# Kernel tuning notes

Measured on AMD Instinct MI355X. Metric: run time of the kernel, lower is better.

The kernel has to match this reference:

```python
import jax, jax.numpy as jnp
import numpy as np
from jax import lax

DX, DY, T, B, NMC, HID = 128, 64, 50, 128, 100, 64
PROC_SD, EMIT_SD, LOC_R = 0.05, 0.1, 5.0


def gaspari_cohn(radius, d):
    # static construction (numpy), matches construct_Gaspari_Cohn
    def G(z):
        if 0 <= z < 1:
            return 1.0 - 5.0/3*z**2 + 5.0/8*z**3 + 0.5*z**4 - 0.25*z**5
        elif 1 <= z < 2:
            return 4.0 - 5.0*z + 5.0/3*z**2 + 5.0/8*z**3 - 0.5*z**4 + 1.0/12*z**5 - 2.0/(3.0*z)
        return 0.0
    t = np.zeros((d, d), dtype=np.float32)
    for i in range(d):
        for j in range(d):
            dist = min(abs(i - j), d - abs(i - j))
            t[i, j] = G(dist / radius)
    return jnp.asarray(t)


def setup_inputs():
    key = jax.random.key(0)
    ks = jax.random.split(key, 16)
    rn = lambda k, s, sc=0.05: (jax.random.normal(k, s) * sc).astype(jnp.float32)
    return {
        'observations': jax.random.normal(ks[0], (B, T, DY), jnp.float32),
        'W1': rn(ks[1], (128, DX)), 'b1': jnp.zeros((128,), jnp.float32),
        'W2': rn(ks[2], (64, 128)), 'b2': jnp.zeros((64,), jnp.float32),
        'W3': rn(ks[3], (32, 64)), 'b3': jnp.zeros((32,), jnp.float32),
        'W4': rn(ks[4], (DX, 32)), 'b4': jnp.zeros((DX,), jnp.float32),
        'Wih': rn(ks[5], (4 * HID, DY)), 'Whh': rn(ks[6], (4 * HID, HID)), 'bih': jnp.zeros((4 * HID,), jnp.float32),
        'Wm': rn(ks[7], (DX, HID)), 'bm': jnp.zeros((DX,), jnp.float32),
        'Wv': rn(ks[8], (DX, HID)), 'bv': jnp.zeros((DX,), jnp.float32),
        'eps0': jax.random.normal(ks[9], (NMC, B, DX), jnp.float32),
        'eps_seq': jax.random.normal(ks[10], (T, NMC, B, DX), jnp.float32),
        'noise_y': jax.random.normal(ks[11], (T, B, DY), jnp.float32),
    }


def _forward(observations, W1, b1, W2, b2, W3, b3, W4, b4,
             Wih, Whh, bih, Wm, bm, Wv, bv, eps0, eps_seq, noise_y):
    dt = observations.dtype
    taper = gaspari_cohn(LOC_R, DX).astype(dt)        # [dx, dx]
    Hm = jnp.eye(DX, dtype=dt)[:DY]                    # [dy, dx] emission matrix
    R = (EMIT_SD ** 2) * jnp.eye(DY, dtype=dt)         # observation noise cov

    def mlp(x):  # Four_Layer_NN, relu, no residual
        h = jax.nn.relu(x @ W1.T + b1)
        h = jax.nn.relu(h @ W2.T + b2)
        h = jax.nn.relu(h @ W3.T + b3)
        return h @ W4.T + b4

    # ---- LSTM recognition net -> q(x0) (diagonal MVN) ----
    def lstm_step(carry, x_t):
        h, c = carry
        g = x_t @ Wih.T + h @ Whh.T + bih
        i, f, gg, o = jnp.split(g, 4, axis=-1)
        c = jax.nn.sigmoid(f) * c + jax.nn.sigmoid(i) * jnp.tanh(gg)
        h = jax.nn.sigmoid(o) * jnp.tanh(c)
        return (h, c), None
    h0 = jnp.zeros((B, HID), dt)
    (h_last, _), _ = lax.scan(lstm_step, (h0, h0), jnp.moveaxis(observations, 1, 0))
    q_mean = h_last @ Wm.T + bm                          # [B, dx]
    q_var = jax.nn.softplus(h_last @ Wv.T + bv) + 1e-4   # [B, dx]

    # KL[ q(x0) || N(0, I) ], diagonal covariance
    kl = 0.5 * jnp.sum(q_var + q_mean ** 2 - 1.0 - jnp.log(q_var), axis=-1).mean()

    # rsample ensemble x0: [NMC, B, dx]
    x0 = q_mean[None] + jnp.sqrt(q_var)[None] * eps0

    log2pi = jnp.log(2 * jnp.asarray(np.pi, dt))

    def enkf_step(x_prev, inp):
        y_t, eps_t, ny_t = inp                            # [B,dy], [NMC,B,dx], [B,dy]
        # NN prediction + process noise
        x_t = mlp(x_prev) + eps_t * PROC_SD               # [NMC, B, dx]
        X = jnp.moveaxis(x_t, 0, 1)                       # [B, NMC, dx]
        Xm = X.mean(axis=1, keepdims=True)                # [B, 1, dx]
        Xc = X - Xm
        # localized ensemble covariance (var_inflation = 0)
        P = taper * (jnp.einsum('bnd,bne->bde', Xc, Xc) / (NMC - 1))  # [B, dx, dx]
        # perturbed observations (chol(R) diagonal)
        y_pert = y_t + ny_t * EMIT_SD                     # [B, dy]
        HX = jnp.einsum('bnd,od->bno', X, Hm)             # [B, NMC, dy]
        HP = jnp.einsum('od,bde->boe', Hm, P)             # [B, dy, dx]
        S = jnp.einsum('boe,pe->bop', HP, Hm) + R         # [B, dy, dy]
        L = jnp.linalg.cholesky(S)
        K = jax.scipy.linalg.cho_solve((L, True), HP)     # [B, dy, dx] = S^-1 HP
        X_post = X + jnp.einsum('bno,boe->bne', y_pert[:, None, :] - HX, K)
        HXm = jnp.einsum('bkd,od->bko', Xm, Hm)           # [B, 1, dy]
        Xm_post = Xm + jnp.einsum('bko,boe->bke', y_t[:, None, :] - HXm, K)
        # EnKF marginal log-likelihood N(y | H Xm, S)
        r = y_t - HXm[:, 0, :]
        z = jax.scipy.linalg.solve_triangular(L, r[..., None], lower=True)[..., 0]
        ll = (-0.5 * jnp.sum(z ** 2, -1)
              - jnp.sum(jnp.log(jnp.diagonal(L, axis1=-2, axis2=-1)), -1)
              - 0.5 * DY * log2pi)
        return jnp.moveaxis(X_post, 0, 1), (ll.mean(), Xm_post[:, 0, :])

    xs = (jnp.moveaxis(observations, 1, 0), eps_seq, noise_y)
    _, (lls, means) = lax.scan(enkf_step, x0, xs)
    elbo = -kl + jnp.sum(lls)
    return elbo, means  # means: [T, B, dx] posterior ensemble means


def reference(observations, W1, b1, W2, b2, W3, b3, W4, b4,
              Wih, Whh, bih, Wm, bm, Wv, bv, eps0, eps_seq, noise_y):
    return _forward(observations, W1, b1, W2, b2, W3, b3, W4, b4,
                    Wih, Whh, bih, Wm, bm, Wv, bv, eps0, eps_seq, noise_y)
```

## Files before the change

### kernel.cpp

```cpp
#include <hip/hip_runtime.h>

#define TC   50
#define BC   128
#define DXC  128
#define DYC  64
#define NMCC 100
#define XBS  136
#define A1S  136
#define A2S  72
#define A3S  40
#define IVS  72
#define KTS  72
#define HPS  20
#define LBS  12
#define ZSS  67
#define W2S  136
#define W3S  72

typedef float f32x4 __attribute__((ext_vector_type(4)));
typedef short s16x8 __attribute__((ext_vector_type(8)));

__device__ __forceinline__ unsigned short f2bf(float x){
  unsigned int u = __float_as_uint(x);
  u += 0x7fffu + ((u >> 16) & 1u);
  return (unsigned short)(u >> 16);
}

__device__ __forceinline__ unsigned int pk2bf(float lo, float hi){
  unsigned int r;
  asm volatile("v_cvt_pk_bf16_f32 %0, %1, %2" : "=v"(r) : "v"(lo), "v"(hi));
  return r;
}

__device__ __forceinline__ f32x4 mfma16(s16x8 a, s16x8 b, f32x4 c){
  return __builtin_amdgcn_mfma_f32_16x16x32_bf16(a, b, c, 0, 0, 0);
}

__device__ __forceinline__ s16x8 packA8(const float* p){
  f32x4 a = *(const f32x4*)p;
  f32x4 c = *(const f32x4*)(p + 4);
  s16x8 r;
  r[0]=(short)f2bf(a[0]); r[1]=(short)f2bf(a[1]);
  r[2]=(short)f2bf(a[2]); r[3]=(short)f2bf(a[3]);
  r[4]=(short)f2bf(c[0]); r[5]=(short)f2bf(c[1]);
  r[6]=(short)f2bf(c[2]); r[7]=(short)f2bf(c[3]);
  return r;
}

__device__ __forceinline__ float gc_taper(int row, int col){
  int dd = row - col; if (dd < 0) dd = -dd;
  if (128 - dd < dd) dd = 128 - dd;
  double z = (double)dd / 5.0;
  double g = 0.0;
  if (z < 1.0){
    g = 1.0 - (5.0/3.0)*z*z + (5.0/8.0)*z*z*z + 0.5*z*z*z*z - 0.25*z*z*z*z*z;
  } else if (z < 2.0){
    g = 4.0 - 5.0*z + (5.0/3.0)*z*z + (5.0/8.0)*z*z*z - 0.5*z*z*z*z
        + (1.0/12.0)*z*z*z*z*z - 2.0/(3.0*z);
  }
  return (float)(g / 99.0);
}

__global__ __launch_bounds__(256) void gin_kernel(const float* __restrict__ obs,
                          const float* __restrict__ Wih, const float* __restrict__ bih,
                          float* __restrict__ gin){
  __shared__ float xrow[64];
  int blk = blockIdx.x;
  int t = blk / BC, b = blk % BC;
  int tid = threadIdx.x;
  if (tid < 64) xrow[tid] = obs[(b*TC + t)*DYC + tid];
  __syncthreads();
  float s = bih[tid];
  #pragma unroll
  for (int k = 0; k < 64; k += 4){
    f32x4 wv = *(const f32x4*)&Wih[tid*64 + k];
    s += wv[0]*xrow[k] + wv[1]*xrow[k+1] + wv[2]*xrow[k+2] + wv[3]*xrow[k+3];
  }
  gin[blk*256 + tid] = s;
}

__global__ __launch_bounds__(256,1) void lstm_kernel(const float* __restrict__ gin,
     const float* __restrict__ Whh,
     const float* __restrict__ Wm, const float* __restrict__ bm,
     const float* __restrict__ Wv, const float* __restrict__ bv,
     float* __restrict__ qmean, float* __restrict__ qstd, float* __restrict__ klp){
  __shared__ float h[64], cc[64], graw[256], red[128];
  int b = blockIdx.x, tid = threadIdx.x;
  float w[64];
  #pragma unroll
  for (int k = 0; k < 64; k += 4){
    f32x4 v = *(const f32x4*)&Whh[tid*64 + k];
    w[k]=v[0]; w[k+1]=v[1]; w[k+2]=v[2]; w[k+3]=v[3];
  }
  if (tid < 64){ h[tid] = 0.f; cc[tid] = 0.f; }
  __syncthreads();
  for (int t = 0; t < TC; ++t){
    float g = gin[(t*BC + b)*256 + tid];
    #pragma unroll
    for (int k = 0; k < 64; k += 4){
      f32x4 hv = *(const f32x4*)&h[k];
      g += hv[0]*w[k] + hv[1]*w[k+1] + hv[2]*w[k+2] + hv[3]*w[k+3];
    }
    graw[tid] = g;
    __syncthreads();
    if (tid < 64){
      float ig = 1.f/(1.f + expf(-graw[tid]));
      float fg = 1.f/(1.f + expf(-graw[64 + tid]));
      float gg = tanhf(graw[128 + tid]);
      float og = 1.f/(1.f + expf(-graw[192 + tid]));
      float cn = fg*cc[tid] + ig*gg;
      cc[tid] = cn;
      h[tid] = og*tanhf(cn);
    }
    __syncthreads();
  }
  if (tid < 128){
    float sm_ = bm[tid], sv_ = bv[tid];
    #pragma unroll
    for (int k = 0; k < 64; k += 4){
      f32x4 wmv = *(const f32x4*)&Wm[tid*64 + k];
      f32x4 wvv = *(const f32x4*)&Wv[tid*64 + k];
      f32x4 hv  = *(const f32x4*)&h[k];
      sm_ += wmv[0]*hv[0] + wmv[1]*hv[1] + wmv[2]*hv[2] + wmv[3]*hv[3];
      sv_ += wvv[0]*hv[0] + wvv[1]*hv[1] + wvv[2]*hv[2] + wvv[3]*hv[3];
    }
    float qv = ((sv_ > 20.f) ? sv_ : log1pf(expf(sv_))) + 1e-4f;
    qmean[b*DXC + tid] = sm_;
    qstd[b*DXC + tid]  = sqrtf(qv);
    red[tid] = 0.5f*(qv + sm_*sm_ - 1.f - logf(qv));
  }
  __syncthreads();
  if (tid == 0){
    float s = 0.f;
    for (int i = 0; i < 128; ++i) s += red[i];
    klp[b] = s;
  }
}

__global__ __launch_bounds__(512,1) void enkf_kernel(
    const float* __restrict__ obs,
    const float* __restrict__ W1, const float* __restrict__ b1g,
    const float* __restrict__ W2, const float* __restrict__ b2g,
    const float* __restrict__ W3, const float* __restrict__ b3g,
    const float* __restrict__ W4, const float* __restrict__ b4g,
    const float* __restrict__ eps0, const float* __restrict__ epss,
    const float* __restrict__ nsyg,
    const float* __restrict__ qmean, const float* __restrict__ qstd,
    float* __restrict__ out_means, float* __restrict__ llp)
{
  __shared__ unsigned short sU[128*XBS];
  __shared__ unsigned short sA[112*A1S];
  __shared__ unsigned short sB[112*A2S];
  __shared__ unsigned short sC[112*A3S];
  __shared__ unsigned short sW2[64*W2S];
  __shared__ unsigned short sW3[32*W3S];
  __shared__ float sHPb[64*HPS];
  __shared__ float sW9[9*12];
  __shared__ float sLb[64*LBS];
  __shared__ float sXm[DXC];
  __shared__ float sRv[DYC];
  __shared__ float sSc[4];

  const int b    = blockIdx.x;
  const int tid  = threadIdx.x;
  const int lane = tid & 63;
  const int wid  = tid >> 6;
  const int l15  = lane & 15;
  const int l4   = lane >> 4;

  const int colN = wid*16 + l15;
  const int rw   = wid;

  s16x8 w1f[4], w4f;
  #pragma unroll
  for (int kt = 0; kt < 4; ++kt) w1f[kt] = packA8(&W1[colN*128 + kt*32 + 8*l4]);
  w4f = packA8(&W4[colN*32 + 8*l4]);
  const float bb1 = b1g[colN], bb4 = b4g[colN];
  float bb2v[4], bb3v[2];
  #pragma unroll
  for (int cg = 0; cg < 4; ++cg) bb2v[cg] = b2g[cg*16 + l15];
  #pragma unroll
  for (int cg = 0; cg < 2; ++cg) bb3v[cg] = b3g[cg*16 + l15];

  const int mt1 = (0x22111000u >> (4*wid)) & 15;
  const int nt1 = (0x21210710u >> (4*wid)) & 15;
  const int mt2 = (0x3332u >> (4*wid)) & 15;
  const int nt2 = (0x4323u >> (4*wid)) & 15;
  float tv1[4], tv2[4];
  #pragma unroll
  for (int i = 0; i < 4; ++i){
    tv1[i] = gc_taper(mt1*16 + 4*l4 + i, nt1*16 + l15);
    tv2[i] = (wid < 4) ? gc_taper(mt2*16 + 4*l4 + i, nt2*16 + l15) : 0.f;
  }

  int cdk = 10, cdd = 0;
  { int acc = 0;
    #pragma unroll
    for (int q = 0; q < 10; ++q){
      int cnt = 10 - q;
      if (lane >= acc && lane < acc + cnt){ cdk = q; cdd = lane - acc; }
      acc += cnt;
    } }
  const int ioff_s  = (cdk + cdd > 9) ? 0 : (cdk + cdd);
  const int dk_s    = (cdk > 9) ? 0 : cdk;
  int baseNext = (cdk + 1)*10 - ((cdk + 1)*cdk)/2;
  const int shsrc   = (baseNext + cdd >= 55) ? 0 : (baseNext + cdd);
  const bool enterSlot = (cdk + cdd == 9) && (cdk <= 9);
  const bool isCol0    = (cdk == 0);

  for (int idx = tid; idx < 64*128; idx += 512)
    sW2[(idx >> 7)*W2S + (idx & 127)] = f2bf(W2[idx]);
  for (int idx = tid; idx < 32*64; idx += 512)
    sW3[(idx >> 6)*W3S + (idx & 63)] = f2bf(W3[idx]);

  float xreg[7][4];
  {
    float qm = qmean[b*DXC + colN], qs = qstd[b*DXC + colN];
    #pragma unroll
    for (int m = 0; m < 7; ++m)
      #pragma unroll
      for (int i = 0; i < 4; ++i){
        int row = m*16 + 4*l4 + i;
        float v = 0.f;
        if (row < NMCC) v = qm + qs * eps0[((size_t)row*BC + b)*DXC + colN];
        xreg[m][i] = v;
        if (row < NMCC) sU[row*XBS + colN] = f2bf(v);
      }
    for (int idx = tid; idx < 12*128; idx += 512)
      sU[(100 + (idx >> 7))*XBS + (idx & 127)] = 0;
  }
  __syncthreads();

  float llsum = 0.f;
  const f32x4 z4 = {0.f, 0.f, 0.f, 0.f};

  for (int t = 0; t < TC; ++t){
    float ldet_t = 0.f;

    float y_r = 0.f, ypv = 0.f;
    if (wid < 4){
      y_r = obs[((size_t)b*TC + t)*DYC + colN];
      ypv = y_r + 0.1f*nsyg[((size_t)t*BC + b)*DYC + colN];
    }

    float ev[7][4];
    #pragma unroll
    for (int m = 0; m < 7; ++m)
      #pragma unroll
      for (int i = 0; i < 4; ++i){
        int row = m*16 + 4*l4 + i;
        ev[m][i] = (row < NMCC)
          ? epss[((size_t)(t*NMCC + row)*BC + b)*DXC + colN] : 0.f;
      }

    {
      f32x4 acc[7];
      #pragma unroll
      for (int m = 0; m < 7; ++m) acc[m] = z4;
      #pragma unroll
      for (int kt = 0; kt < 4; ++kt){
        #pragma unroll
        for (int m = 0; m < 7; ++m){
          s16x8 af = *(const s16x8*)&sU[(m*16 + l15)*XBS + kt*32 + 8*l4];
          acc[m] = mfma16(af, w1f[kt], acc[m]);
        }
      }
      #pragma unroll
      for (int m = 0; m < 7; ++m)
        #pragma unroll
        for (int i = 0; i < 4; ++i){
          int row = m*16 + 4*l4 + i;
          sA[row*A1S + colN] = f2bf(fmaxf(acc[m][i] + bb1, 0.f));
        }
    }
    __syncthreads();

    if (rw < 7){
      f32x4 a2[4];
      #pragma unroll
      for (int cg = 0; cg < 4; ++cg) a2[cg] = z4;
      #pragma unroll
      for (int kt = 0; kt < 4; ++kt){
        s16x8 af = *(const s16x8*)&sA[(16*rw + l15)*A1S + kt*32 + 8*l4];
        #pragma unroll
        for (int cg = 0; cg < 4; ++cg){
          s16x8 bf = *(const s16x8*)&sW2[(cg*16 + l15)*W2S + kt*32 + 8*l4];
          a2[cg] = mfma16(af, bf, a2[cg]);
        }
      }
      #pragma unroll
      for (int cg = 0; cg < 4; ++cg)
        #pragma unroll
        for (int i = 0; i < 4; ++i){
          int row = 16*rw + 4*l4 + i;
          sB[row*A2S + cg*16 + l15] = f2bf(fmaxf(a2[cg][i] + bb2v[cg], 0.f));
        }
      f32x4 a3[2];
      a3[0] = z4; a3[1] = z4;
      #pragma unroll
      for (int kt = 0; kt < 2; ++kt){
        s16x8 af3 = *(const s16x8*)&sB[(16*rw + l15)*A2S + kt*32 + 8*l4];
        #pragma unroll
        for (int cg = 0; cg < 2; ++cg){
          s16x8 bf = *(const s16x8*)&sW3[(cg*16 + l15)*W3S + kt*32 + 8*l4];
          a3[cg] = mfma16(af3, bf, a3[cg]);
        }
      }
      #pragma unroll
      for (int cg = 0; cg < 2; ++cg)
        #pragma unroll
        for (int i = 0; i < 4; ++i){
          int row = 16*rw + 4*l4 + i;
          sC[row*A3S + cg*16 + l15] = f2bf(fmaxf(a3[cg][i] + bb3v[cg], 0.f));
        }
    }
    __syncthreads();

    {
      f32x4 acc[7];
      #pragma unroll
      for (int m = 0; m < 7; ++m) acc[m] = z4;
      #pragma unroll
      for (int m = 0; m < 7; ++m){
        s16x8 af = *(const s16x8*)&sC[(m*16 + l15)*A3S + 8*l4];
        acc[m] = mfma16(af, w4f, acc[m]);
      }
      float part = 0.f;
      #pragma unroll
      for (int m = 0; m < 7; ++m)
        #pragma unroll
        for (int i = 0; i < 4; ++i){
          int row = m*16 + 4*l4 + i;
          if (row < NMCC){
            float v = acc[m][i] + bb4 + 0.05f*ev[m][i];
            xreg[m][i] = v;
            part += v;
          } else xreg[m][i] = 0.f;
        }
      part += __shfl_xor(part, 16);
      part += __shfl_xor(part, 32);
      float xm = part * 0.01f;
      if (l4 == 0) sXm[colN] = xm;
      if (wid < 4 && l4 == 0) sRv[colN] = y_r - xm;

      if (colN <= 72 || colN >= 119){
        #pragma unroll
        for (int m = 0; m < 7; ++m){
          float v0, v1, v2, v3;
          if (m == 6 && l4 > 0){ v0 = v1 = v2 = v3 = 0.f; }
          else {
            v0 = xreg[m][0] - xm; v1 = xreg[m][1] - xm;
            v2 = xreg[m][2] - xm; v3 = xreg[m][3] - xm;
          }
          uint2 pk;
          pk.x = pk2bf(v0, v1);
          pk.y = pk2bf(v2, v3);
          *(uint2*)&sU[colN*XBS + m*16 + 4*l4] = pk;
        }
        uint2 zz; zz.x = 0u; zz.y = 0u;
        *(uint2*)&sU[colN*XBS + 112 + 4*l4] = zz;
      }
      if (wid == 0){
        #pragma unroll
        for (int m = 0; m < 7; ++m)
          #pragma unroll
          for (int i = 0; i < 4; ++i){
            int row = m*16 + 4*l4 + i;
            sB[row*IVS + colN] = (row < NMCC) ? f2bf(ypv - xreg[m][i])
                                              : (unsigned short)0;
          }
      }
    }
    __syncthreads();

    {
      f32x4 a1 = z4, a2 = z4;
      #pragma unroll
      for (int kt = 0; kt < 4; ++kt){
        s16x8 fa1 = *(const s16x8*)&sU[(mt1*16 + l15)*XBS + kt*32 + 8*l4];
        s16x8 fb1 = *(const s16x8*)&sU[(nt1*16 + l15)*XBS + kt*32 + 8*l4];
        a1 = mfma16(fa1, fb1, a1);
        if (wid < 4){
          s16x8 fa2 = *(const s16x8*)&sU[(mt2*16 + l15)*XBS + kt*32 + 8*l4];
          s16x8 fb2 = *(const s16x8*)&sU[(nt2*16 + l15)*XBS + kt*32 + 8*l4];
          a2 = mfma16(fa2, fb2, a2);
        }
      }
      #pragma unroll
      for (int i = 0; i < 4; ++i){
        int o = mt1*16 + 4*l4 + i, e = nt1*16 + l15;
        float v = a1[i] * tv1[i];
        if (nt1 != 7){
          int dd = e - o;
          if (dd >= -9 && dd <= 9) sHPb[o*HPS + dd + 9] = v;
        } else {
          int w = e - 119;
          if (w >= 0 && o <= w) sW9[o*12 + w] = v;
        }
      }
      if (wid < 4){
        #pragma unroll
        for (int i = 0; i < 4; ++i){
          int o = mt2*16 + 4*l4 + i, e = nt2*16 + l15;
          float v = a2[i] * tv2[i];
          int dd = e - o;
          if (dd >= -9 && dd <= 9) sHPb[o*HPS + dd + 9] = v;
        }
      }
    }
    __syncthreads();

    if (wid == 0){
      __builtin_amdgcn_s_setprio(1);
      float v = 0.f;
      if (cdk <= 9) v = sHPb[cdk*HPS + cdd + 9] + ((cdd == 0) ? 0.01f : 0.f);
      for (int j = 0; j < 64; ++j){
        float enter = 0.f;
        if (enterSlot && (j + 10 < 64))
          enter = sHPb[(j + 10 - cdd)*HPS + cdd + 9] + ((cdd == 0) ? 0.01f : 0.f);
        float upiv = __shfl(v, 0);
        float u1   = __shfl(v, ioff_s);
        float u2   = __shfl(v, dk_s);
        float rd   = rsqrtf(upiv);
        float rpiv = rd * rd;
        if (isCol0){
          sLb[j*LBS + cdd] = (cdd == 0) ? rd : v * rd;
        }
        if (lane == 0) ldet_t += 0.5f * logf(upiv);
        float vu = (cdk >= 1) ? v - u1*u2*rpiv : v;
        float vs = __shfl(vu, shsrc);
        v = enterSlot ? enter : vs;
      }
      __builtin_amdgcn_s_setprio(0);
    } else if (wid < 4){
      #pragma unroll
      for (int m = 0; m < 7; ++m)
        #pragma unroll
        for (int i = 0; i < 4; ++i){
          int row = m*16 + 4*l4 + i;
          sB[row*IVS + colN] = (row < NMCC) ? f2bf(ypv - xreg[m][i])
                                            : (unsigned short)0;
        }
    }
    __syncthreads();

    {
      float* zscr = (float*)sU;
      unsigned short* KT = (unsigned short*)sA;
      int c = tid;
      if (c < 83){
        int e = (c < 73) ? c : (c + 46);
        bool isr = (c == 82);
        float w0,w1,w2,w3,w4,w5,w6,w7,w8,w9;
        {
          float wi[10];
          #pragma unroll
          for (int d = 0; d < 10; ++d){
            float bv = 0.f;
            if (isr) bv = sRv[d];
            else if (c < 73){
              int idx = e - d + 9;
              if (idx >= 0 && idx <= 18) bv = sHPb[d*HPS + idx];
            } else {
              int ww = e - 119;
              if (d <= ww) bv = sW9[d*12 + ww];
            }
            wi[d] = bv;
          }
          w0=wi[0]; w1=wi[1]; w2=wi[2]; w3=wi[3]; w4=wi[4];
          w5=wi[5]; w6=wi[6]; w7=wi[7]; w8=wi[8]; w9=wi[9];
        }
        float z2l = 0.f;
        f32x4 lb0 = *(const f32x4*)&sLb[0];
        f32x4 lb4 = *(const f32x4*)&sLb[4];
        float2 l89 = *(const float2*)&sLb[8];
        for (int j = 0; j < 64; ++j){
          f32x4 nb0 = lb0, nb4 = lb4; float2 n89 = l89;
          if (j + 1 < 64){
            nb0 = *(const f32x4*)&sLb[(j+1)*LBS];
            nb4 = *(const f32x4*)&sLb[(j+1)*LBS + 4];
            n89 = *(const float2*)&sLb[(j+1)*LBS + 8];
          }
          float z = w0 * lb0[0];
          zscr[c*ZSS + j] = z;
          z2l += z*z;
          w0 = w1 - lb0[1]*z; w1 = w2 - lb0[2]*z; w2 = w3 - lb0[3]*z;
          w3 = w4 - lb4[0]*z; w4 = w5 - lb4[1]*z; w5 = w6 - lb4[2]*z;
          w6 = w7 - lb4[3]*z; w7 = w8 - l89.x*z;  w8 = w9 - l89.y*z;
          int jn = j + 10;
          float bv = 0.f;
          if (isr){ if (jn < 64) bv = sRv[jn]; }
          else if (c < 73){
            if (jn < 64 && j >= e - 19 && j <= e - 1) bv = sHPb[jn*HPS + (e - j - 1)];
          }
          w9 = bv;
          lb0 = nb0; lb4 = nb4; l89 = n89;
        }
        if (isr) sSc[0] = z2l;
        float x1=0.f,x2=0.f,x3=0.f,x4=0.f,x5=0.f,x6=0.f,x7=0.f,x8=0.f,x9=0.f;
        float macc = 0.f, xodd = 0.f;
        lb0 = *(const f32x4*)&sLb[63*LBS];
        lb4 = *(const f32x4*)&sLb[63*LBS + 4];
        l89 = *(const float2*)&sLb[63*LBS + 8];
        float zcur = zscr[c*ZSS + 63];
        for (int j = 63; j >= 0; --j){
          f32x4 nb0 = lb0, nb4 = lb4; float2 n89 = l89;
          float znext = zcur;
          if (j > 0){
            nb0 = *(const f32x4*)&sLb[(j-1)*LBS];
            nb4 = *(const f32x4*)&sLb[(j-1)*LBS + 4];
            n89 = *(const float2*)&sLb[(j-1)*LBS + 8];
            znext = zscr[c*ZSS + j - 1];
          }
          float acc = zcur
            - lb0[1]*x1 - lb0[2]*x2 - lb0[3]*x3
            - lb4[0]*x4 - lb4[1]*x5 - lb4[2]*x6 - lb4[3]*x7
            - l89.x*x8 - l89.y*x9;
          float xj = acc * lb0[0];
          if (!isr){
            macc += sRv[j]*xj;
            if (j & 1) xodd = xj;
            else *(unsigned int*)&KT[e*KTS + j] = pk2bf(xj, xodd);
          }
          x9=x8; x8=x7; x7=x6; x6=x5; x5=x4; x4=x3; x3=x2; x2=x1; x1=xj;
          lb0 = nb0; lb4 = nb4; l89 = n89; zcur = znext;
        }
        if (!isr) out_means[((size_t)t*BC + b)*DXC + e] = sXm[e] + macc;
      } else if (c < 129){
        int e = c - 10;
        out_means[((size_t)t*BC + b)*DXC + e] = sXm[e];
      }
    }
    __syncthreads();

    if (tid == 0){
      llsum += -0.5f*sSc[0] - ldet_t - 58.812066f;
    }
    {
      f32x4 uacc[7];
      #pragma unroll
      for (int m = 0; m < 7; ++m) uacc[m] = z4;
      if (wid != 5 && wid != 6){
        const unsigned short* KT = (const unsigned short*)sA;
        #pragma unroll
        for (int kt = 0; kt < 2; ++kt){
          s16x8 bf = *(const s16x8*)&KT[colN*KTS + kt*32 + 8*l4];
          #pragma unroll
          for (int m = 0; m < 7; ++m){
            s16x8 af = *(const s16x8*)&sB[(m*16 + l15)*IVS + kt*32 + 8*l4];
            uacc[m] = mfma16(af, bf, uacc[m]);
          }
        }
      }
      bool upd = ((colN <= 72) || (colN >= 119)) && (wid != 5) && (wid != 6);
      #pragma unroll
      for (int m = 0; m < 7; ++m)
        #pragma unroll
        for (int i = 0; i < 4; ++i){
          int row = m*16 + 4*l4 + i;
          if (row < NMCC){
            float xn = xreg[m][i] + (upd ? uacc[m][i] : 0.f);
            xreg[m][i] = xn;
            sU[row*XBS + colN] = f2bf(xn);
          }
        }
    }
    __syncthreads();
  }

  if (tid == 0) llp[b] = llsum;
}

__global__ void final_kernel(const float* __restrict__ klp, const float* __restrict__ llp,
                             float* __restrict__ out){
  __shared__ float s1[128], s2[128];
  int tid = threadIdx.x;
  s1[tid] = klp[tid];
  s2[tid] = llp[tid];
  __syncthreads();
  if (tid == 0){
    float a = 0.f, c = 0.f;
    for (int i = 0; i < 128; ++i){ a += s1[i]; c += s2[i]; }
    out[0] = -a/128.f + c/128.f;
  }
}

extern "C" void kernel_launch(void* const* d_in, const int* in_sizes, int n_in,
                              void* d_out, int out_size, void* d_ws, size_t ws_size,
                              hipStream_t stream){
  (void)in_sizes; (void)n_in; (void)out_size; (void)ws_size;
  const float* obs  = (const float*)d_in[0];
  const float* W1   = (const float*)d_in[1];
  const float* b1   = (const float*)d_in[2];
  const float* W2   = (const float*)d_in[3];
  const float* b2   = (const float*)d_in[4];
  const float* W3   = (const float*)d_in[5];
  const float* b3   = (const float*)d_in[6];
  const float* W4   = (const float*)d_in[7];
  const float* b4   = (const float*)d_in[8];
  const float* Wih  = (const float*)d_in[9];
  const float* Whh  = (const float*)d_in[10];
  const float* bih  = (const float*)d_in[11];
  const float* Wm   = (const float*)d_in[12];
  const float* bm   = (const float*)d_in[13];
  const float* Wv   = (const float*)d_in[14];
  const float* bv   = (const float*)d_in[15];
  const float* eps0 = (const float*)d_in[16];
  const float* epss = (const float*)d_in[17];
  const float* nsy  = (const float*)d_in[18];

  char* ws = (char*)d_ws;
  float* gin   = (float*)(ws + 0);
  float* qmean = (float*)(ws + 6553600);
  float* qstd  = (float*)(ws + 6619136);
  float* klp   = (float*)(ws + 6684672);
  float* llp   = (float*)(ws + 6685184);

  float* out = (float*)d_out;

  hipLaunchKernelGGL(gin_kernel, dim3(TC*BC), dim3(256), 0, stream,
                     obs, Wih, bih, gin);
  hipLaunchKernelGGL(lstm_kernel, dim3(BC), dim3(256), 0, stream,
                     gin, Whh, Wm, bm, Wv, bv, qmean, qstd, klp);
  hipLaunchKernelGGL(enkf_kernel, dim3(BC), dim3(512), 0, stream,
                     obs, W1, b1, W2, b2, W3, b3, W4, b4,
                     eps0, epss, nsy, qmean, qstd, out + 1, llp);
  hipLaunchKernelGGL(final_kernel, dim3(1), dim3(128), 0, stream, klp, llp, out);
}
```

Baseline: 2.041 ms.

## Split banded solve across waves so each wave owns its K rows, drop barrier

The per-step banded forward/back substitution for the gain matrix is redistributed. Each of waves 0-4 and 7 now computes exactly the K^T rows it later consumes in its own MFMA update, and wave 6 handles the residual solve for the log-likelihood. That lets the __syncthreads between the solve and the ensemble update be removed. Forward loops skip the known-zero leading rows of each column, and the z scratch moves to a dedicated shared buffer, since sU is now written concurrently. Log-likelihood accumulation is deferred one step, and a readlane replaces a shuffle for the pivot broadcast. The cost is extra shared memory and more intricate ownership logic.

```diff
diff --git a/kernel.cpp b/kernel.cpp
--- a/kernel.cpp
+++ b/kernel.cpp
@@ -157,6 +157,7 @@
   __shared__ float sHPb[64*HPS];
   __shared__ float sW9[9*12];
   __shared__ float sLb[64*LBS];
+  __shared__ float sZ[83*ZSS];
   __shared__ float sXm[DXC];
   __shared__ float sRv[DYC];
   __shared__ float sSc[4];
@@ -232,10 +233,12 @@
   __syncthreads();
 
   float llsum = 0.f;
+  float pldet = 0.f;
   const f32x4 z4 = {0.f, 0.f, 0.f, 0.f};
 
   for (int t = 0; t < TC; ++t){
-    float ldet_t = 0.f;
+    if (tid == 0 && t > 0)
+      llsum += -0.5f*sSc[0] - pldet - 58.812066f;
 
     float y_r = 0.f, ypv = 0.f;
     if (wid < 4){
@@ -418,7 +421,7 @@
         float enter = 0.f;
         if (enterSlot && (j + 10 < 64))
           enter = sHPb[(j + 10 - cdd)*HPS + cdd + 9] + ((cdd == 0) ? 0.01f : 0.f);
-        float upiv = __shfl(v, 0);
+        float upiv = __uint_as_float(__builtin_amdgcn_readlane(__float_as_uint(v), 0));
         float u1   = __shfl(v, ioff_s);
         float u2   = __shfl(v, dk_s);
         float rd   = rsqrtf(upiv);
@@ -426,7 +429,7 @@
         if (isCol0){
           sLb[j*LBS + cdd] = (cdd == 0) ? rd : v * rd;
         }
-        if (lane == 0) ldet_t += 0.5f * logf(upiv);
+        if (lane == 0) pldet = (j == 0 ? 0.f : pldet) + 0.5f * logf(upiv);
         float vu = (cdk >= 1) ? v - u1*u2*rpiv : v;
         float vs = __shfl(vu, shsrc);
         v = enterSlot ? enter : vs;
@@ -441,107 +444,175 @@
           sB[row*IVS + colN] = (row < NMCC) ? f2bf(ypv - xreg[m][i])
                                             : (unsigned short)0;
         }
+    } else if (wid == 4){
+      if (lane < 46){
+        int e = 73 + lane;
+        out_means[((size_t)t*BC + b)*DXC + e] = sXm[e];
+      }
     }
     __syncthreads();
 
     {
-      float* zscr = (float*)sU;
       unsigned short* KT = (unsigned short*)sA;
-      int c = tid;
-      if (c < 83){
-        int e = (c < 73) ? c : (c + 46);
-        bool isr = (c == 82);
-        float w0,w1,w2,w3,w4,w5,w6,w7,w8,w9;
-        {
-          float wi[10];
-          #pragma unroll
-          for (int d = 0; d < 10; ++d){
-            float bv = 0.f;
-            if (isr) bv = sRv[d];
-            else if (c < 73){
-              int idx = e - d + 9;
-              if (idx >= 0 && idx <= 18) bv = sHPb[d*HPS + idx];
-            } else {
-              int ww = e - 119;
-              if (d <= ww) bv = sW9[d*12 + ww];
+
+      if (wid <= 4){
+        const int E0   = 16*wid;
+        const int nact = (wid == 4) ? 9 : 16;
+        const int j0w  = (E0 >= 9) ? (E0 - 9) : 0;
+        int jR = E0 + 14; if (jR > 53) jR = 53;
+        if (jR < j0w) jR = j0w - 1;
+        if (lane < nact){
+          const int e = E0 + lane;
+          float w0,w1,w2,w3,w4,w5,w6,w7,w8,w9;
+          {
+            float wi[10];
+            #pragma unroll
+            for (int d = 0; d < 10; ++d){
+              int row = j0w + d;
+              int idx = e - row + 9;
+              wi[d] = (row < 64 && idx >= 0 && idx <= 18)
+                      ? sHPb[row*HPS + idx] : 0.f;
             }
-            wi[d] = bv;
-          }
-          w0=wi[0]; w1=wi[1]; w2=wi[2]; w3=wi[3]; w4=wi[4];
-          w5=wi[5]; w6=wi[6]; w7=wi[7]; w8=wi[8]; w9=wi[9];
-        }
-        float z2l = 0.f;
-        f32x4 lb0 = *(const f32x4*)&sLb[0];
-        f32x4 lb4 = *(const f32x4*)&sLb[4];
-        float2 l89 = *(const float2*)&sLb[8];
-        for (int j = 0; j < 64; ++j){
-          f32x4 nb0 = lb0, nb4 = lb4; float2 n89 = l89;
-          if (j + 1 < 64){
-            nb0 = *(const f32x4*)&sLb[(j+1)*LBS];
-            nb4 = *(const f32x4*)&sLb[(j+1)*LBS + 4];
-            n89 = *(const float2*)&sLb[(j+1)*LBS + 8];
-          }
-          float z = w0 * lb0[0];
-          zscr[c*ZSS + j] = z;
-          z2l += z*z;
-          w0 = w1 - lb0[1]*z; w1 = w2 - lb0[2]*z; w2 = w3 - lb0[3]*z;
-          w3 = w4 - lb4[0]*z; w4 = w5 - lb4[1]*z; w5 = w6 - lb4[2]*z;
-          w6 = w7 - lb4[3]*z; w7 = w8 - l89.x*z;  w8 = w9 - l89.y*z;
-          int jn = j + 10;
-          float bv = 0.f;
-          if (isr){ if (jn < 64) bv = sRv[jn]; }
-          else if (c < 73){
-            if (jn < 64 && j >= e - 19 && j <= e - 1) bv = sHPb[jn*HPS + (e - j - 1)];
-          }
-          w9 = bv;
-          lb0 = nb0; lb4 = nb4; l89 = n89;
-        }
-        if (isr) sSc[0] = z2l;
-        float x1=0.f,x2=0.f,x3=0.f,x4=0.f,x5=0.f,x6=0.f,x7=0.f,x8=0.f,x9=0.f;
-        float macc = 0.f, xodd = 0.f;
-        lb0 = *(const f32x4*)&sLb[63*LBS];
-        lb4 = *(const f32x4*)&sLb[63*LBS + 4];
-        l89 = *(const float2*)&sLb[63*LBS + 8];
-        float zcur = zscr[c*ZSS + 63];
-        for (int j = 63; j >= 0; --j){
-          f32x4 nb0 = lb0, nb4 = lb4; float2 n89 = l89;
-          float znext = zcur;
-          if (j > 0){
-            nb0 = *(const f32x4*)&sLb[(j-1)*LBS];
-            nb4 = *(const f32x4*)&sLb[(j-1)*LBS + 4];
-            n89 = *(const float2*)&sLb[(j-1)*LBS + 8];
-            znext = zscr[c*ZSS + j - 1];
-          }
-          float acc = zcur
-            - lb0[1]*x1 - lb0[2]*x2 - lb0[3]*x3
-            - lb4[0]*x4 - lb4[1]*x5 - lb4[2]*x6 - lb4[3]*x7
-            - l89.x*x8 - l89.y*x9;
-          float xj = acc * lb0[0];
-          if (!isr){
+            w0=wi[0]; w1=wi[1]; w2=wi[2]; w3=wi[3]; w4=wi[4];
+            w5=wi[5]; w6=wi[6]; w7=wi[7]; w8=wi[8]; w9=wi[9];
+          }
+          for (int j = j0w; j <= jR; ++j){
+            f32x4 lb0 = *(const f32x4*)&sLb[j*LBS];
+            f32x4 lb4 = *(const f32x4*)&sLb[j*LBS + 4];
+            float2 l89 = *(const float2*)&sLb[j*LBS + 8];
+            float z = w0 * lb0[0];
+            sZ[e*ZSS + j] = z;
+            w0 = w1 - lb0[1]*z; w1 = w2 - lb0[2]*z; w2 = w3 - lb0[3]*z;
+            w3 = w4 - lb4[0]*z; w4 = w5 - lb4[1]*z; w5 = w6 - lb4[2]*z;
+            w6 = w7 - lb4[3]*z; w7 = w8 - l89.x*z;  w8 = w9 - l89.y*z;
+            w9 = (j >= e - 19 && j <= e - 1) ? sHPb[(j+10)*HPS + (e - j - 1)] : 0.f;
+          }
+          for (int j = jR + 1; j < 64; ++j){
+            f32x4 lb0 = *(const f32x4*)&sLb[j*LBS];
+            f32x4 lb4 = *(const f32x4*)&sLb[j*LBS + 4];
+            float2 l89 = *(const float2*)&sLb[j*LBS + 8];
+            float z = w0 * lb0[0];
+            sZ[e*ZSS + j] = z;
+            w0 = w1 - lb0[1]*z; w1 = w2 - lb0[2]*z; w2 = w3 - lb0[3]*z;
+            w3 = w4 - lb4[0]*z; w4 = w5 - lb4[1]*z; w5 = w6 - lb4[2]*z;
+            w6 = w7 - lb4[3]*z; w7 = w8 - l89.x*z;  w8 = w9 - l89.y*z;
+            w9 = 0.f;
+          }
+          float x1=0.f,x2=0.f,x3=0.f,x4=0.f,x5=0.f,x6=0.f,x7=0.f,x8=0.f,x9=0.f;
+          float macc = 0.f, xodd = 0.f;
+          for (int j = 63; j >= j0w; --j){
+            f32x4 lb0 = *(const f32x4*)&sLb[j*LBS];
+            f32x4 lb4 = *(const f32x4*)&sLb[j*LBS + 4];
+            float2 l89 = *(const float2*)&sLb[j*LBS + 8];
+            float acc = sZ[e*ZSS + j]
+              - lb0[1]*x1 - lb0[2]*x2 - lb0[3]*x3
+              - lb4[0]*x4 - lb4[1]*x5 - lb4[2]*x6 - lb4[3]*x7
+              - l89.x*x8 - l89.y*x9;
+            float xj = acc * lb0[0];
             macc += sRv[j]*xj;
             if (j & 1) xodd = xj;
             else *(unsigned int*)&KT[e*KTS + j] = pk2bf(xj, xodd);
-          }
-          x9=x8; x8=x7; x7=x6; x6=x5; x5=x4; x4=x3; x3=x2; x2=x1; x1=xj;
-          lb0 = nb0; lb4 = nb4; l89 = n89; zcur = znext;
-        }
-        if (!isr) out_means[((size_t)t*BC + b)*DXC + e] = sXm[e] + macc;
-      } else if (c < 129){
-        int e = c - 10;
-        out_means[((size_t)t*BC + b)*DXC + e] = sXm[e];
-      }
-    }
-    __syncthreads();
-
-    if (tid == 0){
-      llsum += -0.5f*sSc[0] - ldet_t - 58.812066f;
-    }
-    {
+            x9=x8; x8=x7; x7=x6; x6=x5; x5=x4; x4=x3; x3=x2; x2=x1; x1=xj;
+          }
+          for (int j = j0w - 1; j >= 0; --j){
+            f32x4 lb0 = *(const f32x4*)&sLb[j*LBS];
+            f32x4 lb4 = *(const f32x4*)&sLb[j*LBS + 4];
+            float2 l89 = *(const float2*)&sLb[j*LBS + 8];
+            float acc =
+              - lb0[1]*x1 - lb0[2]*x2 - lb0[3]*x3
+              - lb4[0]*x4 - lb4[1]*x5 - lb4[2]*x6 - lb4[3]*x7
+              - l89.x*x8 - l89.y*x9;
+            float xj = acc * lb0[0];
+            macc += sRv[j]*xj;
+            if (j & 1) xodd = xj;
+            else *(unsigned int*)&KT[e*KTS + j] = pk2bf(xj, xodd);
+            x9=x8; x8=x7; x7=x6; x6=x5; x5=x4; x4=x3; x3=x2; x2=x1; x1=xj;
+          }
+          out_means[((size_t)t*BC + b)*DXC + e] = sXm[e] + macc;
+        }
+        if (wid == 4 && lane >= 9 && lane < 16){
+          int e = 64 + lane;
+          #pragma unroll
+          for (int k = 0; k < 64; k += 8){
+            uint4 zz; zz.x = zz.y = zz.z = zz.w = 0u;
+            *(uint4*)&KT[e*KTS + k] = zz;
+          }
+        }
+      } else if (wid == 7){
+        if (lane < 9){
+          const int e = 119 + lane;
+          const int slot = 73 + lane;
+          float w0,w1,w2,w3,w4,w5,w6,w7,w8,w9;
+          {
+            float wi[10];
+            #pragma unroll
+            for (int d = 0; d < 10; ++d)
+              wi[d] = (d <= lane) ? sW9[d*12 + lane] : 0.f;
+            w0=wi[0]; w1=wi[1]; w2=wi[2]; w3=wi[3]; w4=wi[4];
+            w5=wi[5]; w6=wi[6]; w7=wi[7]; w8=wi[8]; w9=wi[9];
+          }
+          for (int j = 0; j < 64; ++j){
+            f32x4 lb0 = *(const f32x4*)&sLb[j*LBS];
+            f32x4 lb4 = *(const f32x4*)&sLb[j*LBS + 4];
+            float2 l89 = *(const float2*)&sLb[j*LBS + 8];
+            float z = w0 * lb0[0];
+            sZ[slot*ZSS + j] = z;
+            w0 = w1 - lb0[1]*z; w1 = w2 - lb0[2]*z; w2 = w3 - lb0[3]*z;
+            w3 = w4 - lb4[0]*z; w4 = w5 - lb4[1]*z; w5 = w6 - lb4[2]*z;
+            w6 = w7 - lb4[3]*z; w7 = w8 - l89.x*z;  w8 = w9 - l89.y*z;
+            w9 = 0.f;
+          }
+          float x1=0.f,x2=0.f,x3=0.f,x4=0.f,x5=0.f,x6=0.f,x7=0.f,x8=0.f,x9=0.f;
+          float macc = 0.f, xodd = 0.f;
+          for (int j = 63; j >= 0; --j){
+            f32x4 lb0 = *(const f32x4*)&sLb[j*LBS];
+            f32x4 lb4 = *(const f32x4*)&sLb[j*LBS + 4];
+            float2 l89 = *(const float2*)&sLb[j*LBS + 8];
+            float acc = sZ[slot*ZSS + j]
+              - lb0[1]*x1 - lb0[2]*x2 - lb0[3]*x3
+              - lb4[0]*x4 - lb4[1]*x5 - lb4[2]*x6 - lb4[3]*x7
+              - l89.x*x8 - l89.y*x9;
+            float xj = acc * lb0[0];
+            macc += sRv[j]*xj;
+            if (j & 1) xodd = xj;
+            else *(unsigned int*)&KT[e*KTS + j] = pk2bf(xj, xodd);
+            x9=x8; x8=x7; x7=x6; x6=x5; x5=x4; x4=x3; x3=x2; x2=x1; x1=xj;
+          }
+          out_means[((size_t)t*BC + b)*DXC + e] = sXm[e] + macc;
+        }
+        if (lane >= 9 && lane < 16){
+          int e = 103 + lane;
+          #pragma unroll
+          for (int k = 0; k < 64; k += 8){
+            uint4 zz; zz.x = zz.y = zz.z = zz.w = 0u;
+            *(uint4*)&KT[e*KTS + k] = zz;
+          }
+        }
+      } else if (wid == 6){
+        if (lane == 0){
+          float w0,w1,w2,w3,w4,w5,w6,w7,w8,w9;
+          w0=sRv[0]; w1=sRv[1]; w2=sRv[2]; w3=sRv[3]; w4=sRv[4];
+          w5=sRv[5]; w6=sRv[6]; w7=sRv[7]; w8=sRv[8]; w9=sRv[9];
+          float z2l = 0.f;
+          for (int j = 0; j < 64; ++j){
+            f32x4 lb0 = *(const f32x4*)&sLb[j*LBS];
+            f32x4 lb4 = *(const f32x4*)&sLb[j*LBS + 4];
+            float2 l89 = *(const float2*)&sLb[j*LBS + 8];
+            float z = w0 * lb0[0];
+            z2l += z*z;
+            w0 = w1 - lb0[1]*z; w1 = w2 - lb0[2]*z; w2 = w3 - lb0[3]*z;
+            w3 = w4 - lb4[0]*z; w4 = w5 - lb4[1]*z; w5 = w6 - lb4[2]*z;
+            w6 = w7 - lb4[3]*z; w7 = w8 - l89.x*z;  w8 = w9 - l89.y*z;
+            w9 = (j + 10 < 64) ? sRv[j + 10] : 0.f;
+          }
+          sSc[0] = z2l;
+        }
+      }
+
       f32x4 uacc[7];
       #pragma unroll
       for (int m = 0; m < 7; ++m) uacc[m] = z4;
       if (wid != 5 && wid != 6){
-        const unsigned short* KT = (const unsigned short*)sA;
         #pragma unroll
         for (int kt = 0; kt < 2; ++kt){
           s16x8 bf = *(const s16x8*)&KT[colN*KTS + kt*32 + 8*l4];
@@ -552,14 +623,13 @@
           }
         }
       }
-      bool upd = ((colN <= 72) || (colN >= 119)) && (wid != 5) && (wid != 6);
       #pragma unroll
       for (int m = 0; m < 7; ++m)
         #pragma unroll
         for (int i = 0; i < 4; ++i){
           int row = m*16 + 4*l4 + i;
           if (row < NMCC){
-            float xn = xreg[m][i] + (upd ? uacc[m][i] : 0.f);
+            float xn = xreg[m][i] + uacc[m][i];
             xreg[m][i] = xn;
             sU[row*XBS + colN] = f2bf(xn);
           }
@@ -568,7 +638,10 @@
     __syncthreads();
   }
 
-  if (tid == 0) llp[b] = llsum;
+  if (tid == 0){
+    llsum += -0.5f*sSc[0] - pldet - 58.812066f;
+    llp[b] = llsum;
+  }
 }
 
 __global__ void final_kernel(const float* __restrict__ klp, const float* __restrict__ llp,
```

Result: faster. 1.760 ms (-13.8%).
